# Optimization experiments

Hardware: AMD Instinct MI355X
Metric: run time of the kernel (lower is better)

Reference implementation:

```python
import jax, jax.numpy as jnp
import numpy as np

STRIDE = 1
PADDING = 0


def setup_inputs() -> dict:
    key = jax.random.key(0)
    k1, k2, k3 = jax.random.split(key, 3)
    B, E, Cin, Cout, H, W = 32, 8, 64, 64, 160, 160
    x = jax.random.normal(k1, (B, Cin, H, W), dtype=jnp.float32)
    alpha = jax.random.uniform(k2, (B, E), dtype=jnp.float32)
    kernel_embed = jax.random.normal(k3, (E, Cout, Cin, 1, 1), dtype=jnp.float32)
    return {"x": x, "alpha": alpha, "kernel_embed": kernel_embed}


def reference(x, alpha, kernel_embed):
    # Per-sample kernel mix: [B,E] x [E,O,I,kh,kw] -> [B,O,I,kh,kw]
    kernels = jnp.einsum('be,eoihw->boihw', alpha, kernel_embed)

    def conv_one(xi, ki):
        # xi: [Cin,H,W], ki: [Cout,Cin,kh,kw]
        out = jax.lax.conv_general_dilated(
            xi[None],  # [1,Cin,H,W]
            ki,
            window_strides=(STRIDE, STRIDE),
            padding=[(PADDING, PADDING), (PADDING, PADDING)],
            dimension_numbers=('NCHW', 'OIHW', 'NCHW'),
        )
        return out[0]  # [Cout,Ho,Wo]

    return jax.vmap(conv_one)(x, kernels)  # [B,Cout,Ho,Wo]
```

## Files before the change

kernel.cpp:

```cpp
#include <hip/hip_runtime.h>
#include <cstdint>
#include <cstddef>


#define PIX 25600
#define CIN 64
#define COUT 64
#define BATCH 32
#define NEXP 8
#define TILE_PX 128
#define TILES_PER_B (PIX / TILE_PX)
#define TPB 5
#define GROUPS (TILES_PER_B / TPB)

__device__ __forceinline__ void load_lds16(const float* g, float* l) {
  __builtin_amdgcn_global_load_lds(
      (__attribute__((address_space(1))) void*)(g),
      (__attribute__((address_space(3))) void*)(l), 16, 0, 0);
}

__global__ __launch_bounds__(256) void mix_kernel(
    const float* __restrict__ alpha, const float* __restrict__ ke,
    float* __restrict__ kt) {
  const int b = blockIdx.x >> 3;
  const int seg = blockIdx.x & 7;
  __shared__ float a[NEXP];
  if (threadIdx.x < NEXP) a[threadIdx.x] = alpha[b * NEXP + threadIdx.x];
  __syncthreads();
#pragma unroll
  for (int t = 0; t < 2; t++) {
    const int idx = seg * 512 + t * 256 + threadIdx.x;
    float s = 0.f;
#pragma unroll
    for (int e = 0; e < NEXP; e++) s += a[e] * ke[e * 4096 + idx];
    const int o = idx >> 6, i = idx & 63;
    kt[b * 4096 + i * 64 + o] = s;
  }
}

__global__ __launch_bounds__(256, 2) void conv_kernel(
    const float* __restrict__ x, const float* __restrict__ kt,
    float* __restrict__ out) {
  __shared__ float ks[CIN * COUT];
  __shared__ float xs[2][CIN * TILE_PX];

  const int bid = blockIdx.x;
  const int b = bid / GROUPS;
  const int g = bid - b * GROUPS;
  const int tile0 = g * TPB;

  const int tid = threadIdx.x;
  const int wave = tid >> 6;
  const int lane = tid & 63;
  const int tc = tid >> 5;
  const int tp = tid & 31;

  const float* xb = x + (size_t)b * CIN * PIX;
  const float* kb = kt + b * 4096;

#pragma unroll
  for (int j = 0; j < 4; j++) {
    const int r = wave * 4 + j;
    load_lds16(kb + r * 256 + lane * 4, &ks[r * 256]);
  }

  {
    const float* gs = xb + (size_t)tile0 * TILE_PX;
#pragma unroll
    for (int j = 0; j < 8; j++) {
      const int r = wave * 16 + j * 2;
      load_lds16(gs + (size_t)(r + (lane >> 5)) * PIX + (lane & 31) * 4,
                 &xs[0][r * TILE_PX]);
    }
  }

  for (int t = 0; t < TPB; ++t) {
    const int cur = t & 1;

    if (t) {
      __builtin_amdgcn_s_barrier();
      asm volatile("" ::: "memory");
    }

    if (t + 1 < TPB) {
      const float* gs = xb + (size_t)(tile0 + t + 1) * TILE_PX;
      float* dst = xs[cur ^ 1];
#pragma unroll
      for (int j = 0; j < 8; j++) {
        const int r = wave * 16 + j * 2;
        load_lds16(gs + (size_t)(r + (lane >> 5)) * PIX + (lane & 31) * 4,
                   dst + r * TILE_PX);
      }
    }

    if (t == 0 || t + 1 == TPB) {
      asm volatile("s_waitcnt vmcnt(8)" ::: "memory");
    } else {
      asm volatile("s_waitcnt vmcnt(16)" ::: "memory");
    }
    __builtin_amdgcn_s_barrier();

    float acc[8][4];
#pragma unroll
    for (int c = 0; c < 8; c++)
#pragma unroll
      for (int p = 0; p < 4; p++) acc[c][p] = 0.f;

    const float* xp4 = &xs[cur][tp * 4];
    const float* kp = ks + tc * 8;
#pragma unroll 8
    for (int ii = 0; ii < CIN; ii++) {
      const float4 xv = *(const float4*)(xp4 + ii * TILE_PX);
      const float4 k0 = *(const float4*)(kp + ii * 64);
      const float4 k1 = *(const float4*)(kp + ii * 64 + 4);
      const float kc[8] = {k0.x, k0.y, k0.z, k0.w, k1.x, k1.y, k1.z, k1.w};
      const float xv4[4] = {xv.x, xv.y, xv.z, xv.w};
#pragma unroll
      for (int c = 0; c < 8; c++)
#pragma unroll
        for (int p = 0; p < 4; p++) acc[c][p] = fmaf(kc[c], xv4[p], acc[c][p]);
    }

    float* ob = out + ((size_t)(b * COUT + tc * 8)) * PIX +
                (size_t)(tile0 + t) * TILE_PX + tp * 4;
#pragma unroll
    for (int c = 0; c < 8; c++) {
      *(float4*)(ob + (size_t)c * PIX) =
          make_float4(acc[c][0], acc[c][1], acc[c][2], acc[c][3]);
    }
  }
}

extern "C" void kernel_launch(void* const* d_in, const int* in_sizes, int n_in,
                              void* d_out, int out_size, void* d_ws,
                              size_t ws_size, hipStream_t stream) {
  const float* x = (const float*)d_in[0];
  const float* alpha = (const float*)d_in[1];
  const float* ke = (const float*)d_in[2];
  float* out = (float*)d_out;
  float* kt = (float*)d_ws;

  mix_kernel<<<BATCH * 8, 256, 0, stream>>>(alpha, ke, kt);
  conv_kernel<<<BATCH * GROUPS, 256, 0, stream>>>(x, kt, out);
}
```

Before: 378.2 us.

## Use persistent grid-stride tiles and read wave-uniform weights via scalar loads

The conv kernel now launches a fixed grid of 512 blocks that stride over all batch-tile pairs, instead of one block per group of five tiles within a batch. The weights are no longer staged in LDS. Each wave owns 16 output channels and reads the weights with wave-uniform addresses, which should allow scalar loads, while each lane computes 2 pixels. The aim is to cut LDS traffic and weight staging, and to balance work across CUs. In exchange, weights are re-read from global or cache on every tile, and the per-iteration wait counts have to be tuned.

```diff
diff --git a/kernel.cpp b/kernel.cpp
--- a/kernel.cpp
+++ b/kernel.cpp
@@ -10,8 +10,8 @@
 #define NEXP 8
 #define TILE_PX 128
 #define TILES_PER_B (PIX / TILE_PX)
-#define TPB 5
-#define GROUPS (TILES_PER_B / TPB)
+#define TOT_TILES (BATCH * TILES_PER_B)
+#define GRID 512
 
 __device__ __forceinline__ void load_lds16(const float* g, float* l) {
   __builtin_amdgcn_global_load_lds(
@@ -41,31 +41,18 @@
 __global__ __launch_bounds__(256, 2) void conv_kernel(
     const float* __restrict__ x, const float* __restrict__ kt,
     float* __restrict__ out) {
-  __shared__ float ks[CIN * COUT];
   __shared__ float xs[2][CIN * TILE_PX];
 
   const int bid = blockIdx.x;
-  const int b = bid / GROUPS;
-  const int g = bid - b * GROUPS;
-  const int tile0 = g * TPB;
-
   const int tid = threadIdx.x;
   const int wave = tid >> 6;
   const int lane = tid & 63;
-  const int tc = tid >> 5;
-  const int tp = tid & 31;
-
-  const float* xb = x + (size_t)b * CIN * PIX;
-  const float* kb = kt + b * 4096;
-
-#pragma unroll
-  for (int j = 0; j < 4; j++) {
-    const int r = wave * 4 + j;
-    load_lds16(kb + r * 256 + lane * 4, &ks[r * 256]);
-  }
+  const int wu = __builtin_amdgcn_readfirstlane(wave);
 
   {
-    const float* gs = xb + (size_t)tile0 * TILE_PX;
+    const int b0 = bid / TILES_PER_B;
+    const int tl0 = bid - b0 * TILES_PER_B;
+    const float* gs = x + (size_t)b0 * CIN * PIX + (size_t)tl0 * TILE_PX;
 #pragma unroll
     for (int j = 0; j < 8; j++) {
       const int r = wave * 16 + j * 2;
@@ -74,16 +61,22 @@
     }
   }
 
-  for (int t = 0; t < TPB; ++t) {
-    const int cur = t & 1;
+  int cur = 0;
+  for (int t = bid; t < TOT_TILES; t += GRID) {
+    const int b = t / TILES_PER_B;
+    const int tl = t - b * TILES_PER_B;
+    const int tn = t + GRID;
+    const bool has_next = (tn < TOT_TILES);
 
-    if (t) {
+    if (t != bid) {
       __builtin_amdgcn_s_barrier();
       asm volatile("" ::: "memory");
     }
 
-    if (t + 1 < TPB) {
-      const float* gs = xb + (size_t)(tile0 + t + 1) * TILE_PX;
+    if (has_next) {
+      const int bn = tn / TILES_PER_B;
+      const int tln = tn - bn * TILES_PER_B;
+      const float* gs = x + (size_t)bn * CIN * PIX + (size_t)tln * TILE_PX;
       float* dst = xs[cur ^ 1];
 #pragma unroll
       for (int j = 0; j < 8; j++) {
@@ -93,41 +86,51 @@
       }
     }
 
-    if (t == 0 || t + 1 == TPB) {
-      asm volatile("s_waitcnt vmcnt(8)" ::: "memory");
+    if (t == bid) {
+      if (has_next) {
+        asm volatile("s_waitcnt vmcnt(8)" ::: "memory");
+      } else {
+        asm volatile("s_waitcnt vmcnt(0)" ::: "memory");
+      }
     } else {
-      asm volatile("s_waitcnt vmcnt(16)" ::: "memory");
+      if (has_next) {
+        asm volatile("s_waitcnt vmcnt(24)" ::: "memory");
+      } else {
+        asm volatile("s_waitcnt vmcnt(16)" ::: "memory");
+      }
     }
     __builtin_amdgcn_s_barrier();
+    asm volatile("" ::: "memory");
 
-    float acc[8][4];
+    float acc[16][2];
 #pragma unroll
-    for (int c = 0; c < 8; c++)
-#pragma unroll
-      for (int p = 0; p < 4; p++) acc[c][p] = 0.f;
-
-    const float* xp4 = &xs[cur][tp * 4];
-    const float* kp = ks + tc * 8;
-#pragma unroll 8
-    for (int ii = 0; ii < CIN; ii++) {
-      const float4 xv = *(const float4*)(xp4 + ii * TILE_PX);
-      const float4 k0 = *(const float4*)(kp + ii * 64);
-      const float4 k1 = *(const float4*)(kp + ii * 64 + 4);
-      const float kc[8] = {k0.x, k0.y, k0.z, k0.w, k1.x, k1.y, k1.z, k1.w};
-      const float xv4[4] = {xv.x, xv.y, xv.z, xv.w};
-#pragma unroll
-      for (int c = 0; c < 8; c++)
-#pragma unroll
-        for (int p = 0; p < 4; p++) acc[c][p] = fmaf(kc[c], xv4[p], acc[c][p]);
+    for (int c = 0; c < 16; c++) {
+      acc[c][0] = 0.f;
+      acc[c][1] = 0.f;
     }
 
-    float* ob = out + ((size_t)(b * COUT + tc * 8)) * PIX +
-                (size_t)(tile0 + t) * TILE_PX + tp * 4;
+    const float* kb = kt + b * 4096 + wu * 16;
+    const float* xp = &xs[cur][lane * 2];
+#pragma unroll 4
+    for (int ii = 0; ii < CIN; ii++) {
+      const float2 xv = *(const float2*)(xp + ii * TILE_PX);
+      const float* kr = kb + ii * 64;
 #pragma unroll
-    for (int c = 0; c < 8; c++) {
-      *(float4*)(ob + (size_t)c * PIX) =
-          make_float4(acc[c][0], acc[c][1], acc[c][2], acc[c][3]);
+      for (int c = 0; c < 16; c++) {
+        const float kv = kr[c];
+        acc[c][0] = fmaf(kv, xv.x, acc[c][0]);
+        acc[c][1] = fmaf(kv, xv.y, acc[c][1]);
+      }
     }
+
+    float* ob = out + ((size_t)(b * COUT + wu * 16)) * PIX +
+                (size_t)tl * TILE_PX + lane * 2;
+#pragma unroll
+    for (int c = 0; c < 16; c++) {
+      *(float2*)(ob + (size_t)c * PIX) = make_float2(acc[c][0], acc[c][1]);
+    }
+
+    cur ^= 1;
   }
 }
 
@@ -141,5 +144,5 @@
   float* kt = (float*)d_ws;
 
   mix_kernel<<<BATCH * 8, 256, 0, stream>>>(alpha, ke, kt);
-  conv_kernel<<<BATCH * GROUPS, 256, 0, stream>>>(x, kt, out);
+  conv_kernel<<<GRID, 256, 0, stream>>>(x, kt, out);
 }
```

Measured after the change: 389.1 us. 1.03x slower.
